# Kernel optimization log

Hardware: AMD Instinct MI355X
Metric: run time of the kernel (lower is better)

The kernel has to match this reference:

```python
import jax, jax.numpy as jnp
import numpy as np

B, L, H = 32, 2048, 512


def setup_inputs() -> dict:
    key = jax.random.key(0)
    k1, k2, k3, k4, k5, k6 = jax.random.split(key, 6)
    scale = 1.0 / np.sqrt(H)
    return {
        "query": jax.random.normal(k1, (B, H), dtype=jnp.float32),
        "ref": jax.random.normal(k2, (B, L, H), dtype=jnp.float32),
        "mask": jax.random.randint(k3, (B, L), 0, 2) == 1,
        # learned params (torch Linear weight layout: [out, in]; apply as x @ W.T)
        "W_ref": jax.random.normal(k4, (H, H), dtype=jnp.float32) * scale,
        "W_q": jax.random.normal(k5, (H, H), dtype=jnp.float32) * scale,
        "v": jax.random.normal(k6, (H,), dtype=jnp.float32) * scale,
    }


def reference(query, ref, mask, W_ref, W_q, v):
    scale = 1.0 / np.sqrt(H)
    # additive (Bahdanau) scores: v^T tanh(W_ref ref + W_q q)
    encoded_ref = jnp.einsum("blh,oh->blo", ref, W_ref)          # (B, L, H)
    encoded_q = jnp.einsum("bh,oh->bo", query, W_q)[:, None, :]  # (B, 1, H)
    scores = jnp.einsum("blh,h->bl", jnp.tanh(encoded_ref + encoded_q), v)
    scores = scores * scale
    scores = jnp.where(mask, -1e9, scores)
    attn = jax.nn.softmax(scores, axis=1)                         # (B, L)
    glimpse = jnp.einsum("bl,blh->bh", attn, ref)                 # (B, H)
    return glimpse, scores
```

## Files before the change

kernel.cpp:

```cpp
#include <hip/hip_runtime.h>
#include <hip/hip_bf16.h>
#include <cstdint>

typedef __attribute__((ext_vector_type(4))) float f32x4;
typedef __attribute__((ext_vector_type(8))) short s16x8;

#define NB   32
#define NL   2048
#define NH   512
#define NM   (NB * NL)
#define SCALE 0.04419417382415922f
#define LDST 40

__device__ __forceinline__ ushort f2bf(float f) {
    union { float f; unsigned u; } a; a.f = f;
    unsigned u = a.u;
    unsigned r = (u + 0x7FFFu + ((u >> 16) & 1u)) >> 16;
    return (ushort)r;
}

__global__ __launch_bounds__(256) void k_convW(const float* __restrict__ W,
                                               ushort* __restrict__ Wb) {
    int i = blockIdx.x * 256 + threadIdx.x;
    const float4* s = (const float4*)W;
    float4 a = s[2 * i], c = s[2 * i + 1];
    union { ushort u[8]; int4 v; } p;
    p.u[0] = f2bf(a.x); p.u[1] = f2bf(a.y); p.u[2] = f2bf(a.z); p.u[3] = f2bf(a.w);
    p.u[4] = f2bf(c.x); p.u[5] = f2bf(c.y); p.u[6] = f2bf(c.z); p.u[7] = f2bf(c.w);
    ((int4*)Wb)[i] = p.v;
}

__global__ __launch_bounds__(512) void k_eq(const float* __restrict__ query,
                                            const float* __restrict__ Wq,
                                            float* __restrict__ eq) {
    int b = blockIdx.x;
    int o = threadIdx.x;
    __shared__ float q[NH];
    q[o] = query[b * NH + o];
    __syncthreads();
    const float4* w = (const float4*)(Wq + (size_t)o * NH);
    float acc = 0.f;
#pragma unroll 4
    for (int i = 0; i < NH / 4; ++i) {
        float4 x = w[i];
        acc += q[4 * i] * x.x + q[4 * i + 1] * x.y + q[4 * i + 2] * x.z + q[4 * i + 3] * x.w;
    }
    eq[b * NH + o] = acc;
}

__global__ __launch_bounds__(256) void k_gemm(const float* __restrict__ ref,
                                              const ushort* __restrict__ Wb,
                                              const float* __restrict__ eq,
                                              const float* __restrict__ v,
                                              float* __restrict__ part) {
    __shared__ ushort As[128 * LDST];
    __shared__ ushort Bs[128 * LDST];

    int tid = threadIdx.x;
    int lane = tid & 63, wid = tid >> 6;
    int wr = wid >> 1, wc = wid & 1;

    int phys = blockIdx.x;
    int xcd = phys & 7, slot = phys >> 3;
    int mt = xcd * 64 + (slot >> 2);
    int nt = slot & 3;
    int m0 = mt * 128, n0 = nt * 128;
    int b = mt >> 4;

    f32x4 acc[4][4];
#pragma unroll
    for (int i = 0; i < 4; ++i)
#pragma unroll
        for (int j = 0; j < 4; ++j) acc[i][j] = (f32x4)(0.f);

    int srow = tid >> 1, sks = (tid & 1) * 16;
    const float*  asrc = ref + (size_t)(m0 + srow) * NH + sks;
    const ushort* bsrc = Wb + (size_t)(n0 + srow) * NH + sks;
    int awr = srow * LDST + sks;

    int lr = lane & 15, kq = lane >> 4;
    int aoff[4], boff[4];
#pragma unroll
    for (int f = 0; f < 4; ++f) {
        aoff[f] = (wr * 64 + f * 16 + lr) * LDST + kq * 8;
        boff[f] = (wc * 64 + f * 16 + lr) * LDST + kq * 8;
    }

    for (int kt = 0; kt < 16; ++kt) {
        __syncthreads();
        {
            const float* s = asrc + kt * 32;
            float4 f0 = *(const float4*)(s);
            float4 f1 = *(const float4*)(s + 4);
            float4 f2 = *(const float4*)(s + 8);
            float4 f3 = *(const float4*)(s + 12);
            union { ushort u[8]; int4 v; } p0, p1;
            p0.u[0] = f2bf(f0.x); p0.u[1] = f2bf(f0.y); p0.u[2] = f2bf(f0.z); p0.u[3] = f2bf(f0.w);
            p0.u[4] = f2bf(f1.x); p0.u[5] = f2bf(f1.y); p0.u[6] = f2bf(f1.z); p0.u[7] = f2bf(f1.w);
            p1.u[0] = f2bf(f2.x); p1.u[1] = f2bf(f2.y); p1.u[2] = f2bf(f2.z); p1.u[3] = f2bf(f2.w);
            p1.u[4] = f2bf(f3.x); p1.u[5] = f2bf(f3.y); p1.u[6] = f2bf(f3.z); p1.u[7] = f2bf(f3.w);
            *(int4*)&As[awr] = p0.v;
            *(int4*)&As[awr + 8] = p1.v;
            const int4* bs = (const int4*)(bsrc + kt * 32);
            *(int4*)&Bs[awr] = bs[0];
            *(int4*)&Bs[awr + 8] = bs[1];
        }
        __syncthreads();
        s16x8 af[4], bf[4];
#pragma unroll
        for (int f = 0; f < 4; ++f) af[f] = *(const s16x8*)&As[aoff[f]];
#pragma unroll
        for (int f = 0; f < 4; ++f) bf[f] = *(const s16x8*)&Bs[boff[f]];
#pragma unroll
        for (int fr = 0; fr < 4; ++fr)
#pragma unroll
            for (int fc = 0; fc < 4; ++fc)
                acc[fr][fc] = __builtin_amdgcn_mfma_f32_16x16x32_bf16(
                    af[fr], bf[fc], acc[fr][fc], 0, 0, 0);
    }

    const float* eqb = eq + b * NH;
    float vv[4], ee[4];
#pragma unroll
    for (int fc = 0; fc < 4; ++fc) {
        int c = n0 + wc * 64 + fc * 16 + lr;
        vv[fc] = v[c];
        ee[fc] = eqb[c];
    }
#pragma unroll
    for (int fr = 0; fr < 4; ++fr) {
#pragma unroll
        for (int reg = 0; reg < 4; ++reg) {
            float s = 0.f;
#pragma unroll
            for (int fc = 0; fc < 4; ++fc) {
                float x = acc[fr][fc][reg] + ee[fc];
                float t = 1.f - 2.f / (__expf(2.f * x) + 1.f);
                s += vv[fc] * t;
            }
            s += __shfl_xor(s, 1);
            s += __shfl_xor(s, 2);
            s += __shfl_xor(s, 4);
            s += __shfl_xor(s, 8);
            if (lr == 0) {
                int row = wr * 64 + fr * 16 + kq * 4 + reg;
                part[(size_t)nt * NM + m0 + row] = s;
            }
        }
    }
}

__global__ __launch_bounds__(256) void k_softmax(const float* __restrict__ part,
                                                 const int* __restrict__ mask,
                                                 float* __restrict__ out_sc,
                                                 float* __restrict__ attn) {
    int b = blockIdx.x;
    int tid = threadIdx.x;
    int lane = tid & 63, wid = tid >> 6;
    __shared__ float red[4];
    float sc[8];
    float mx = -3.4e38f;
#pragma unroll
    for (int i = 0; i < 8; ++i) {
        int m = b * NL + i * 256 + tid;
        float s = (part[m] + part[NM + m] + part[2 * NM + m] + part[3 * NM + m]) * SCALE;
        if (mask[m] != 0) s = -1e9f;
        out_sc[m] = s;
        sc[i] = s;
        mx = fmaxf(mx, s);
    }
#pragma unroll
    for (int o = 32; o >= 1; o >>= 1) mx = fmaxf(mx, __shfl_xor(mx, o));
    if (lane == 0) red[wid] = mx;
    __syncthreads();
    mx = fmaxf(fmaxf(red[0], red[1]), fmaxf(red[2], red[3]));
    __syncthreads();
    float ls = 0.f;
#pragma unroll
    for (int i = 0; i < 8; ++i) {
        float e = __expf(sc[i] - mx);
        sc[i] = e;
        ls += e;
    }
#pragma unroll
    for (int o = 32; o >= 1; o >>= 1) ls += __shfl_xor(ls, o);
    if (lane == 0) red[wid] = ls;
    __syncthreads();
    float inv = 1.f / (red[0] + red[1] + red[2] + red[3]);
#pragma unroll
    for (int i = 0; i < 8; ++i) attn[b * NL + i * 256 + tid] = sc[i] * inv;
}

__global__ __launch_bounds__(256) void k_glp(const float* __restrict__ ref,
                                             const float* __restrict__ attn,
                                             float* __restrict__ glp) {
    int sp = blockIdx.x, b = blockIdx.y;
    int tid = threadIdx.x;
    const float* attb = attn + b * NL + sp * 128;
    float2 acc = make_float2(0.f, 0.f);
#pragma unroll 4
    for (int l = 0; l < 128; ++l) {
        float a = attb[l];
        const float2* row = (const float2*)(ref + (size_t)(b * NL + sp * 128 + l) * NH);
        float2 r = row[tid];
        acc.x += a * r.x;
        acc.y += a * r.y;
    }
    ((float2*)(glp + (size_t)(sp * NB + b) * NH))[tid] = acc;
}

__global__ __launch_bounds__(256) void k_gred(const float* __restrict__ glp,
                                              float* __restrict__ out_gl) {
    int idx = blockIdx.x * 256 + threadIdx.x;
    float s = 0.f;
#pragma unroll
    for (int sp = 0; sp < 16; ++sp) s += glp[sp * (NB * NH) + idx];
    out_gl[idx] = s;
}

extern "C" void kernel_launch(void* const* d_in, const int* in_sizes, int n_in,
                              void* d_out, int out_size, void* d_ws, size_t ws_size,
                              hipStream_t stream) {
    const float* query = (const float*)d_in[0];
    const float* ref   = (const float*)d_in[1];
    const int*   mask  = (const int*)d_in[2];
    const float* W_ref = (const float*)d_in[3];
    const float* W_q   = (const float*)d_in[4];
    const float* v     = (const float*)d_in[5];

    float* out_gl = (float*)d_out;
    float* out_sc = out_gl + NB * NH;

    char* w = (char*)d_ws;
    ushort* wW  = (ushort*)w;
    float* eq   = (float*)(w + 524288);
    float* part = (float*)(w + 589824);
    float* attn = (float*)(w + 1638400);
    float* glp  = (float*)(w + 1900544);

    k_convW<<<128, 256, 0, stream>>>(W_ref, wW);
    k_eq<<<NB, 512, 0, stream>>>(query, W_q, eq);
    k_gemm<<<2048, 256, 0, stream>>>(ref, wW, eq, v, part);
    k_softmax<<<NB, 256, 0, stream>>>(part, mask, out_sc, attn);
    k_glp<<<dim3(16, NB), 256, 0, stream>>>(ref, attn, glp);
    k_gred<<<64, 256, 0, stream>>>(glp, out_gl);
}
```

Measured before the change: 139.2 us.

## Restructure pipeline: full-N GEMM tiles with double-buffered LDS, fused softmax-glimpse

Each GEMM block now computes a 64-row tile across all 512 output columns, so ref is read and converted once instead of four times. The score reduction, scale and mask now happen in-kernel, which removes the partial-score buffer. W_ref bf16 tiles are staged with global_load_lds into double-buffered LDS, and A is prefetched so loads overlap the MFMAs. The prep kernels are merged into one launch, and the softmax is folded into the glimpse kernel, with each block recomputing the row max and sum. The cost is a large LDS footprint (about 74 KB per block) that may limit occupancy, plus redundant softmax work across the 16 glimpse blocks.

New measurement: 123.2 us. 1.13x faster.

```diff
diff --git a/kernel.cpp b/kernel.cpp
--- a/kernel.cpp
+++ b/kernel.cpp
@@ -10,62 +10,76 @@
 #define NH   512
 #define NM   (NB * NL)
 #define SCALE 0.04419417382415922f
-#define LDST 40
 
 __device__ __forceinline__ ushort f2bf(float f) {
-    union { float f; unsigned u; } a; a.f = f;
-    unsigned u = a.u;
-    unsigned r = (u + 0x7FFFu + ((u >> 16) & 1u)) >> 16;
-    return (ushort)r;
-}
-
-__global__ __launch_bounds__(256) void k_convW(const float* __restrict__ W,
-                                               ushort* __restrict__ Wb) {
-    int i = blockIdx.x * 256 + threadIdx.x;
-    const float4* s = (const float4*)W;
-    float4 a = s[2 * i], c = s[2 * i + 1];
-    union { ushort u[8]; int4 v; } p;
-    p.u[0] = f2bf(a.x); p.u[1] = f2bf(a.y); p.u[2] = f2bf(a.z); p.u[3] = f2bf(a.w);
-    p.u[4] = f2bf(c.x); p.u[5] = f2bf(c.y); p.u[6] = f2bf(c.z); p.u[7] = f2bf(c.w);
-    ((int4*)Wb)[i] = p.v;
-}
-
-__global__ __launch_bounds__(512) void k_eq(const float* __restrict__ query,
-                                            const float* __restrict__ Wq,
-                                            float* __restrict__ eq) {
-    int b = blockIdx.x;
-    int o = threadIdx.x;
-    __shared__ float q[NH];
-    q[o] = query[b * NH + o];
-    __syncthreads();
-    const float4* w = (const float4*)(Wq + (size_t)o * NH);
-    float acc = 0.f;
+    __hip_bfloat16 b = __float2bfloat16(f);
+    return *reinterpret_cast<ushort*>(&b);
+}
+__device__ __forceinline__ unsigned long long pack4(float4 f) {
+    union { ushort u[4]; unsigned long long v; } p;
+    p.u[0] = f2bf(f.x); p.u[1] = f2bf(f.y); p.u[2] = f2bf(f.z); p.u[3] = f2bf(f.w);
+    return p.v;
+}
+
+__device__ __forceinline__ void gl16(const ushort* g, ushort* l) {
+    __builtin_amdgcn_global_load_lds(
+        (const __attribute__((address_space(1))) unsigned int*)g,
+        (__attribute__((address_space(3))) unsigned int*)l,
+        16, 0, 0);
+}
+
+__global__ __launch_bounds__(256) void k_pre(const float* __restrict__ W,
+                                             ushort* __restrict__ Wb,
+                                             const float* __restrict__ query,
+                                             const float* __restrict__ Wq,
+                                             float* __restrict__ eq) {
+    int bid = blockIdx.x;
+    int t = threadIdx.x;
+    if (bid < 64) {
+        const float4* F = (const float4*)W;
+        unsigned long long* U = (unsigned long long*)Wb;
+        int base = bid * 1024 + t;
+        float4 f[4];
+#pragma unroll
+        for (int k = 0; k < 4; ++k) f[k] = F[base + k * 256];
+#pragma unroll
+        for (int k = 0; k < 4; ++k) U[base + k * 256] = pack4(f[k]);
+    } else {
+        __shared__ float q[NH];
+        int b = bid - 64;
+        q[t] = query[b * NH + t];
+        q[t + 256] = query[b * NH + t + 256];
+        __syncthreads();
+#pragma unroll
+        for (int half = 0; half < 2; ++half) {
+            int o = t + half * 256;
+            const float4* w = (const float4*)(Wq + (size_t)o * NH);
+            float acc = 0.f;
 #pragma unroll 4
-    for (int i = 0; i < NH / 4; ++i) {
-        float4 x = w[i];
-        acc += q[4 * i] * x.x + q[4 * i + 1] * x.y + q[4 * i + 2] * x.z + q[4 * i + 3] * x.w;
-    }
-    eq[b * NH + o] = acc;
-}
-
-__global__ __launch_bounds__(256) void k_gemm(const float* __restrict__ ref,
-                                              const ushort* __restrict__ Wb,
-                                              const float* __restrict__ eq,
-                                              const float* __restrict__ v,
-                                              float* __restrict__ part) {
-    __shared__ ushort As[128 * LDST];
-    __shared__ ushort Bs[128 * LDST];
+            for (int i = 0; i < NH / 4; ++i) {
+                float4 x = w[i];
+                acc += q[4 * i] * x.x + q[4 * i + 1] * x.y + q[4 * i + 2] * x.z + q[4 * i + 3] * x.w;
+            }
+            eq[b * NH + o] = acc;
+        }
+    }
+}
+
+__global__ __launch_bounds__(512, 4) void k_gemm_full(const float* __restrict__ ref,
+                                                      const ushort* __restrict__ Wb,
+                                                      const float* __restrict__ eq,
+                                                      const float* __restrict__ v,
+                                                      const int* __restrict__ mask,
+                                                      float* __restrict__ out_sc) {
+    __shared__ ushort Bs[2][512 * 32];
+    __shared__ ushort As[2][64 * 36];
+    __shared__ float sc_red[8][64];
 
     int tid = threadIdx.x;
     int lane = tid & 63, wid = tid >> 6;
-    int wr = wid >> 1, wc = wid & 1;
-
-    int phys = blockIdx.x;
-    int xcd = phys & 7, slot = phys >> 3;
-    int mt = xcd * 64 + (slot >> 2);
-    int nt = slot & 3;
-    int m0 = mt * 128, n0 = nt * 128;
-    int b = mt >> 4;
+    int blk = blockIdx.x;
+    int m0g = blk << 6;
+    int b = blk >> 5;
 
     f32x4 acc[4][4];
 #pragma unroll
@@ -73,57 +87,69 @@
 #pragma unroll
         for (int j = 0; j < 4; ++j) acc[i][j] = (f32x4)(0.f);
 
-    int srow = tid >> 1, sks = (tid & 1) * 16;
-    const float*  asrc = ref + (size_t)(m0 + srow) * NH + sks;
-    const ushort* bsrc = Wb + (size_t)(n0 + srow) * NH + sks;
-    int awr = srow * LDST + sks;
+    const ushort* bglob = Wb + ((size_t)(wid * 64) + (lane >> 2)) * NH + (lane & 3) * 8;
+    int arow = tid >> 3, acol = (tid & 7) * 4;
+    const float* aglob = ref + (size_t)(m0g + arow) * NH + acol;
+    int awr = arow * 36 + acol;
 
     int lr = lane & 15, kq = lane >> 4;
-    int aoff[4], boff[4];
-#pragma unroll
-    for (int f = 0; f < 4; ++f) {
-        aoff[f] = (wr * 64 + f * 16 + lr) * LDST + kq * 8;
-        boff[f] = (wc * 64 + f * 16 + lr) * LDST + kq * 8;
-    }
-
-    for (int kt = 0; kt < 16; ++kt) {
+    int aof = lr * 36 + kq * 8;
+    int bof = (wid * 64 + lr) * 32 + kq * 8;
+
+#define STAGE_B(buf, kt)                                                     \
+    {   gl16(bglob + (kt) * 32,               &Bs[buf][(wid * 64) * 32]);    \
+        gl16(bglob + (kt) * 32 + 16 * NH,     &Bs[buf][(wid * 64 + 16) * 32]); \
+        gl16(bglob + (kt) * 32 + 32 * NH,     &Bs[buf][(wid * 64 + 32) * 32]); \
+        gl16(bglob + (kt) * 32 + 48 * NH,     &Bs[buf][(wid * 64 + 48) * 32]); }
+
+#define LOAD_A(kt)   pa = *(const float4*)(aglob + (kt) * 32);
+
+#define WRITE_A(buf) { *(unsigned long long*)&As[buf][awr] = pack4(pa); }
+
+#define READ_FRAGS(buf)                                                      \
+    _Pragma("unroll")                                                        \
+    for (int f = 0; f < 4; ++f) af[f] = *(const s16x8*)&As[buf][aof + f * 16 * 36]; \
+    _Pragma("unroll")                                                        \
+    for (int f = 0; f < 4; ++f) bfr[f] = *(const s16x8*)&Bs[buf][bof + f * 16 * 32];
+
+#define DO_MFMA()                                                            \
+    _Pragma("unroll")                                                        \
+    for (int fr = 0; fr < 4; ++fr)                                           \
+        _Pragma("unroll")                                                    \
+        for (int fc = 0; fc < 4; ++fc)                                       \
+            acc[fr][fc] = __builtin_amdgcn_mfma_f32_16x16x32_bf16(af[fr], bfr[fc], acc[fr][fc], 0, 0, 0);
+
+    float4 pa;
+    LOAD_A(0)
+    WRITE_A(0)
+    STAGE_B(0, 0)
+    __syncthreads();
+
+    for (int t2 = 0; t2 < 8; ++t2) {
+        s16x8 af[4], bfr[4];
+        int k0 = 2 * t2;
+        if (k0 + 1 < 16) { LOAD_A(k0 + 1) STAGE_B(1, k0 + 1) }
+        READ_FRAGS(0)
+        DO_MFMA()
+        if (k0 + 1 < 16) WRITE_A(1)
         __syncthreads();
-        {
-            const float* s = asrc + kt * 32;
-            float4 f0 = *(const float4*)(s);
-            float4 f1 = *(const float4*)(s + 4);
-            float4 f2 = *(const float4*)(s + 8);
-            float4 f3 = *(const float4*)(s + 12);
-            union { ushort u[8]; int4 v; } p0, p1;
-            p0.u[0] = f2bf(f0.x); p0.u[1] = f2bf(f0.y); p0.u[2] = f2bf(f0.z); p0.u[3] = f2bf(f0.w);
-            p0.u[4] = f2bf(f1.x); p0.u[5] = f2bf(f1.y); p0.u[6] = f2bf(f1.z); p0.u[7] = f2bf(f1.w);
-            p1.u[0] = f2bf(f2.x); p1.u[1] = f2bf(f2.y); p1.u[2] = f2bf(f2.z); p1.u[3] = f2bf(f2.w);
-            p1.u[4] = f2bf(f3.x); p1.u[5] = f2bf(f3.y); p1.u[6] = f2bf(f3.z); p1.u[7] = f2bf(f3.w);
-            *(int4*)&As[awr] = p0.v;
-            *(int4*)&As[awr + 8] = p1.v;
-            const int4* bs = (const int4*)(bsrc + kt * 32);
-            *(int4*)&Bs[awr] = bs[0];
-            *(int4*)&Bs[awr + 8] = bs[1];
-        }
+        if (k0 + 2 < 16) { LOAD_A(k0 + 2) STAGE_B(0, k0 + 2) }
+        READ_FRAGS(1)
+        DO_MFMA()
+        if (k0 + 2 < 16) WRITE_A(0)
         __syncthreads();
-        s16x8 af[4], bf[4];
-#pragma unroll
-        for (int f = 0; f < 4; ++f) af[f] = *(const s16x8*)&As[aoff[f]];
-#pragma unroll
-        for (int f = 0; f < 4; ++f) bf[f] = *(const s16x8*)&Bs[boff[f]];
-#pragma unroll
-        for (int fr = 0; fr < 4; ++fr)
-#pragma unroll
-            for (int fc = 0; fc < 4; ++fc)
-                acc[fr][fc] = __builtin_amdgcn_mfma_f32_16x16x32_bf16(
-                    af[fr], bf[fc], acc[fr][fc], 0, 0, 0);
-    }
+    }
+#undef STAGE_B
+#undef LOAD_A
+#undef WRITE_A
+#undef READ_FRAGS
+#undef DO_MFMA
 
     const float* eqb = eq + b * NH;
     float vv[4], ee[4];
 #pragma unroll
     for (int fc = 0; fc < 4; ++fc) {
-        int c = n0 + wc * 64 + fc * 16 + lr;
+        int c = wid * 64 + fc * 16 + lr;
         vv[fc] = v[c];
         ee[fc] = eqb[c];
     }
@@ -142,32 +168,35 @@
             s += __shfl_xor(s, 2);
             s += __shfl_xor(s, 4);
             s += __shfl_xor(s, 8);
-            if (lr == 0) {
-                int row = wr * 64 + fr * 16 + kq * 4 + reg;
-                part[(size_t)nt * NM + m0 + row] = s;
-            }
+            if (lr == 0) sc_red[wid][fr * 16 + kq * 4 + reg] = s;
         }
     }
-}
-
-__global__ __launch_bounds__(256) void k_softmax(const float* __restrict__ part,
-                                                 const int* __restrict__ mask,
-                                                 float* __restrict__ out_sc,
-                                                 float* __restrict__ attn) {
-    int b = blockIdx.x;
+    __syncthreads();
+    if (tid < 64) {
+        float t = 0.f;
+#pragma unroll
+        for (int w = 0; w < 8; ++w) t += sc_red[w][tid];
+        t *= SCALE;
+        int rg = m0g + tid;
+        if (mask[rg] != 0) t = -1e9f;
+        out_sc[rg] = t;
+    }
+}
+
+__global__ __launch_bounds__(256) void k_smglp(const float* __restrict__ scores,
+                                               const float* __restrict__ ref,
+                                               float* __restrict__ glp) {
+    int sp = blockIdx.x, b = blockIdx.y;
     int tid = threadIdx.x;
     int lane = tid & 63, wid = tid >> 6;
     __shared__ float red[4];
+    __shared__ float asl[128];
     float sc[8];
     float mx = -3.4e38f;
 #pragma unroll
     for (int i = 0; i < 8; ++i) {
-        int m = b * NL + i * 256 + tid;
-        float s = (part[m] + part[NM + m] + part[2 * NM + m] + part[3 * NM + m]) * SCALE;
-        if (mask[m] != 0) s = -1e9f;
-        out_sc[m] = s;
-        sc[i] = s;
-        mx = fmaxf(mx, s);
+        sc[i] = scores[b * NL + i * 256 + tid];
+        mx = fmaxf(mx, sc[i]);
     }
 #pragma unroll
     for (int o = 32; o >= 1; o >>= 1) mx = fmaxf(mx, __shfl_xor(mx, o));
@@ -179,33 +208,26 @@
 #pragma unroll
     for (int i = 0; i < 8; ++i) {
         float e = __expf(sc[i] - mx);
-        sc[i] = e;
         ls += e;
+        if (i == (sp >> 1) && (tid >> 7) == (sp & 1)) asl[tid & 127] = e;
     }
 #pragma unroll
     for (int o = 32; o >= 1; o >>= 1) ls += __shfl_xor(ls, o);
     if (lane == 0) red[wid] = ls;
     __syncthreads();
     float inv = 1.f / (red[0] + red[1] + red[2] + red[3]);
-#pragma unroll
-    for (int i = 0; i < 8; ++i) attn[b * NL + i * 256 + tid] = sc[i] * inv;
-}
-
-__global__ __launch_bounds__(256) void k_glp(const float* __restrict__ ref,
-                                             const float* __restrict__ attn,
-                                             float* __restrict__ glp) {
-    int sp = blockIdx.x, b = blockIdx.y;
-    int tid = threadIdx.x;
-    const float* attb = attn + b * NL + sp * 128;
+
+    const float* rb = ref + ((size_t)b * NL + sp * 128) * NH;
     float2 acc = make_float2(0.f, 0.f);
 #pragma unroll 4
     for (int l = 0; l < 128; ++l) {
-        float a = attb[l];
-        const float2* row = (const float2*)(ref + (size_t)(b * NL + sp * 128 + l) * NH);
-        float2 r = row[tid];
+        float a = asl[l];
+        float2 r = ((const float2*)(rb + (size_t)l * NH))[tid];
         acc.x += a * r.x;
         acc.y += a * r.y;
     }
+    acc.x *= inv;
+    acc.y *= inv;
     ((float2*)(glp + (size_t)(sp * NB + b) * NH))[tid] = acc;
 }
 
@@ -232,16 +254,12 @@
     float* out_sc = out_gl + NB * NH;
 
     char* w = (char*)d_ws;
-    ushort* wW  = (ushort*)w;
-    float* eq   = (float*)(w + 524288);
-    float* part = (float*)(w + 589824);
-    float* attn = (float*)(w + 1638400);
-    float* glp  = (float*)(w + 1900544);
-
-    k_convW<<<128, 256, 0, stream>>>(W_ref, wW);
-    k_eq<<<NB, 512, 0, stream>>>(query, W_q, eq);
-    k_gemm<<<2048, 256, 0, stream>>>(ref, wW, eq, v, part);
-    k_softmax<<<NB, 256, 0, stream>>>(part, mask, out_sc, attn);
-    k_glp<<<dim3(16, NB), 256, 0, stream>>>(ref, attn, glp);
+    ushort* wW = (ushort*)w;
+    float* eq  = (float*)(w + 524288);
+    float* glp = (float*)(w + 589824);
+
+    k_pre<<<96, 256, 0, stream>>>(W_ref, wW, query, W_q, eq);
+    k_gemm_full<<<1024, 512, 0, stream>>>(ref, wW, eq, v, mask, out_sc);
+    k_smglp<<<dim3(16, NB), 256, 0, stream>>>(out_sc, ref, glp);
     k_gred<<<64, 256, 0, stream>>>(glp, out_gl);
 }
```
